# Kernel optimization log

Hardware: AMD Instinct MI355X
Metric: run time of the kernel (lower is better)

## Reference

```python
import jax, jax.numpy as jnp
import numpy as np

N = 200000      # active voxels
K = 27          # kernel volume (3x3x3)
M = 50000       # rulebook pairs per kernel offset
CIN = 64
COUT = 64


def setup_inputs() -> dict:
    key = jax.random.key(0)
    k1, k2, k3, k4 = jax.random.split(key, 4)
    feats = jax.random.normal(k1, (N, CIN), dtype=jnp.float32)
    std = 1.0 / np.sqrt(CIN * K)
    kernel = jax.random.uniform(k2, (K, CIN, COUT), dtype=jnp.float32,
                                minval=-std, maxval=std)
    in_map = jax.random.randint(k3, (K, M), 0, N, dtype=jnp.int32)
    out_map = jax.random.randint(k4, (K, M), 0, N, dtype=jnp.int32)
    return {"feats": feats, "kernel": kernel, "in_map": in_map, "out_map": out_map}


def reference(feats, kernel, in_map, out_map):
    # gather: [K, M, Cin]
    gathered = feats[in_map]
    # per-offset GEMM: [K, M, Cout]
    partial = jnp.einsum('kmi,kio->kmo', gathered, kernel)
    # scatter-add into output features [N, Cout]
    out = jnp.zeros((feats.shape[0], kernel.shape[-1]), dtype=feats.dtype)
    out = out.at[out_map].add(partial)
    return out
```

## Files before the change

kernel.cpp:

```cpp
#include <hip/hip_runtime.h>
#include <hip/hip_fp16.h>

#define CIN   64
#define COUT  64

typedef __attribute__((ext_vector_type(8))) short bf16x8;
typedef __attribute__((ext_vector_type(4))) float f32x4;
typedef __attribute__((ext_vector_type(4))) unsigned u32x4;

__device__ inline unsigned short f2bf(float f) {
    unsigned u = __float_as_uint(f);
    return (unsigned short)((u + 0x7FFFu + ((u >> 16) & 1u)) >> 16);
}

__device__ inline unsigned pack_h2(float lo, float hi) {
    __half l = __float2half(lo), h = __float2half(hi);
    return (unsigned)__half_as_ushort(l) | ((unsigned)__half_as_ushort(h) << 16);
}

__device__ inline float2 h2f2(unsigned v) {
    return make_float2(
        __half2float(__ushort_as_half((unsigned short)(v & 0xFFFFu))),
        __half2float(__ushort_as_half((unsigned short)(v >> 16))));
}

__global__ __launch_bounds__(256)
void cvt_hist(const f32x4* __restrict__ in, unsigned short* __restrict__ outb,
              int n8, const int* __restrict__ out_map, int total,
              int* __restrict__ cnt, int* __restrict__ rk) {
    int i = blockIdx.x * 256 + threadIdx.x;
    if (i < n8) {
        f32x4 f0 = __builtin_nontemporal_load(&in[2 * i]);
        f32x4 f1 = __builtin_nontemporal_load(&in[2 * i + 1]);
        bf16x8 o;
        o[0] = (short)f2bf(f0[0]); o[1] = (short)f2bf(f0[1]);
        o[2] = (short)f2bf(f0[2]); o[3] = (short)f2bf(f0[3]);
        o[4] = (short)f2bf(f1[0]); o[5] = (short)f2bf(f1[1]);
        o[6] = (short)f2bf(f1[2]); o[7] = (short)f2bf(f1[3]);
        *(bf16x8*)(outb + 8 * (size_t)i) = o;
    }
    if (i < total)
        rk[i] = atomicAdd(&cnt[out_map[i]], 1);
}

__global__ __launch_bounds__(256)
void scanA(const int* __restrict__ cnt, int* __restrict__ excl,
           int* __restrict__ blocksum, int N) {
    __shared__ int sm[256];
    const int b = blockIdx.x, t = threadIdx.x;
    const int base = b * 1024 + t * 4;
    int v0 = (base + 0 < N) ? cnt[base + 0] : 0;
    int v1 = (base + 1 < N) ? cnt[base + 1] : 0;
    int v2 = (base + 2 < N) ? cnt[base + 2] : 0;
    int v3 = (base + 3 < N) ? cnt[base + 3] : 0;
    const int s = v0 + v1 + v2 + v3;
    sm[t] = s; __syncthreads();
    for (int off = 1; off < 256; off <<= 1) {
        int x = (t >= off) ? sm[t - off] : 0;
        __syncthreads();
        sm[t] += x;
        __syncthreads();
    }
    const int e = sm[t] - s;
    if (t == 255) blocksum[b] = sm[t];
    if (base + 0 < N) excl[base + 0] = e;
    if (base + 1 < N) excl[base + 1] = e + v0;
    if (base + 2 < N) excl[base + 2] = e + v0 + v1;
    if (base + 3 < N) excl[base + 3] = e + v0 + v1 + v2;
}

__global__ __launch_bounds__(256)
void scanB(const int* __restrict__ blocksum, int* __restrict__ blockbase,
           int nb, int* __restrict__ total_out) {
    __shared__ int sm[256];
    const int t = threadIdx.x;
    const int s = (t < nb) ? blocksum[t] : 0;
    sm[t] = s; __syncthreads();
    for (int off = 1; off < 256; off <<= 1) {
        int x = (t >= off) ? sm[t - off] : 0;
        __syncthreads();
        sm[t] += x;
        __syncthreads();
    }
    if (t < nb) blockbase[t] = sm[t] - s;
    if (t == 255) *total_out = sm[255];
}

__global__ __launch_bounds__(256)
void scanC(int* __restrict__ offsets, const int* __restrict__ blockbase, int N,
           int nblk, const float* __restrict__ weight,
           unsigned short* __restrict__ wb, int kvol) {
    const int b = blockIdx.x;
    if (b < nblk) {
        int i = b * 256 + threadIdx.x;
        if (i < N) offsets[i] += blockbase[i >> 10];
        return;
    }
    const int idx = (b - nblk) * 256 + threadIdx.x;
    if (idx >= kvol * 64 * 8) return;
    const int k   = idx >> 9;
    const int rem = idx & 511;
    const int n   = rem >> 3;
    const int c0  = (rem & 7) << 3;
    const float* __restrict__ wk = weight + (size_t)k * (CIN * COUT);
    unsigned short* __restrict__ dst = wb + ((size_t)k * 64 + n) * 64 + c0;
#pragma unroll
    for (int j = 0; j < 8; ++j)
        dst[j] = f2bf(wk[(c0 + j) * COUT + n]);
}

__global__ __launch_bounds__(256)
void fill_idx(const int* __restrict__ out_map, const int* __restrict__ rk,
              const int* __restrict__ offsets, int* __restrict__ idx,
              int total) {
    int p = blockIdx.x * 256 + threadIdx.x;
    if (p < total)
        idx[offsets[out_map[p]] + rk[p]] = p;
}

__global__ __launch_bounds__(256)
void spconv_phase1(const unsigned short* __restrict__ featsb,
                   const unsigned short* __restrict__ wb,
                   const int*            __restrict__ in_map,
                   unsigned*             __restrict__ partial_dw,
                   int M) {
    const int k      = blockIdx.y;
    const int tid    = threadIdx.x;
    const int lane   = tid & 63;
    const int m      = lane & 15;
    const int quad   = lane >> 4;
    const int wave   = blockIdx.x * 4 + (tid >> 6);
    const int nwaves = gridDim.x * 4;

    const unsigned short* __restrict__ wkb = wb + (size_t)k * (CIN * COUT);
    bf16x8 afrag[4][2];
#pragma unroll
    for (int t = 0; t < 4; ++t) {
        const int n = 16 * (m >> 2) + 4 * t + (m & 3);
#pragma unroll
        for (int h = 0; h < 2; ++h)
            afrag[t][h] = *(const bf16x8*)(wkb + n * 64 + 32 * h + 8 * quad);
    }

    const int base   = k * M;
    const int ntiles = M >> 4;

    int t0 = wave, t1 = wave + nwaves, t2 = wave + 2 * nwaves;

    int ir0 = 0;
    if (t0 < ntiles) ir0 = in_map[base + (t0 << 4) + m];
    bf16x8 a0_0 = {}, a1_0 = {};
    if (t0 < ntiles) {
        const unsigned short* fb = featsb + ((size_t)ir0 << 6) + 8 * quad;
        a0_0 = *(const bf16x8*)fb;
        a1_0 = *(const bf16x8*)(fb + 32);
    }
    int ir1 = 0;
    if (t1 < ntiles) ir1 = in_map[base + (t1 << 4) + m];

    while (t0 < ntiles) {
        bf16x8 a0_1 = {}, a1_1 = {};
        if (t1 < ntiles) {
            const unsigned short* fb = featsb + ((size_t)ir1 << 6) + 8 * quad;
            a0_1 = *(const bf16x8*)fb;
            a1_1 = *(const bf16x8*)(fb + 32);
        }
        int ir2 = 0;
        if (t2 < ntiles) ir2 = in_map[base + (t2 << 4) + m];

        f32x4 acc[4];
#pragma unroll
        for (int t = 0; t < 4; ++t) {
            acc[t] = {0.f, 0.f, 0.f, 0.f};
            acc[t] = __builtin_amdgcn_mfma_f32_16x16x32_bf16(afrag[t][0], a0_0, acc[t], 0, 0, 0);
            acc[t] = __builtin_amdgcn_mfma_f32_16x16x32_bf16(afrag[t][1], a1_0, acc[t], 0, 0, 0);
        }

        const size_t pair = (size_t)base + ((size_t)t0 << 4) + m;
        unsigned d[8];
#pragma unroll
        for (int t = 0; t < 4; ++t) {
            d[2 * t]     = pack_h2(acc[t][0], acc[t][1]);
            d[2 * t + 1] = pack_h2(acc[t][2], acc[t][3]);
        }
        uint4* dst = (uint4*)(partial_dw + pair * 32 + 8 * quad);
        dst[0] = make_uint4(d[0], d[1], d[2], d[3]);
        dst[1] = make_uint4(d[4], d[5], d[6], d[7]);

        t0 = t1; t1 = t2; t2 += nwaves;
        a0_0 = a0_1; a1_0 = a1_1;
        ir1 = ir2;
    }
}

__global__ __launch_bounds__(256)
void spconv_phase2(const u32x4* __restrict__ partial_q,
                   const int*   __restrict__ idx,
                   const int*   __restrict__ offsets,
                   float4*      __restrict__ out4,
                   int nrows) {
    const int tid  = threadIdx.x;
    const int lane = tid & 63;
    const int g    = lane >> 3;
    const int q    = lane & 7;
    const int wave = blockIdx.x * 4 + (tid >> 6);
    const int nw   = gridDim.x * 4;

    for (int r0 = 4 * wave; r0 < nrows; r0 += 4 * nw) {
        const int nr = (nrows - r0 < 4) ? (nrows - r0) : 4;

        int offv[5];
        offv[0] = offsets[r0];
#pragma unroll
        for (int u = 1; u <= 4; ++u)
            offv[u] = (u <= nr) ? offsets[r0 + u] : offv[u - 1];

        int  pj[4];
        bool act[4];
#pragma unroll
        for (int u = 0; u < 4; ++u) {
            const int s = offv[u] + g;
            act[u] = (s < offv[u + 1]);
            pj[u]  = act[u] ? idx[s] : 0;
        }
        u32x4 v[4];
#pragma unroll
        for (int u = 0; u < 4; ++u) {
            v[u] = (u32x4){0u, 0u, 0u, 0u};
            if (act[u]) v[u] = partial_q[(size_t)pj[u] * 8 + q];
        }

        float acc[4][8];
#pragma unroll
        for (int u = 0; u < 4; ++u) {
            const float2 f0 = h2f2(v[u][0]), f1 = h2f2(v[u][1]);
            const float2 f2 = h2f2(v[u][2]), f3 = h2f2(v[u][3]);
            acc[u][0] = f0.x; acc[u][1] = f0.y; acc[u][2] = f1.x; acc[u][3] = f1.y;
            acc[u][4] = f2.x; acc[u][5] = f2.y; acc[u][6] = f3.x; acc[u][7] = f3.y;
        }

#pragma unroll
        for (int u = 0; u < 4; ++u) {
            const int cu = offv[u + 1] - offv[u];
            for (int j0 = 8; j0 < cu; j0 += 8) {
                const int j = j0 + g;
                if (j < cu) {
                    const int pj2 = idx[offv[u] + j];
                    const u32x4 w = partial_q[(size_t)pj2 * 8 + q];
                    const float2 f0 = h2f2(w[0]), f1 = h2f2(w[1]);
                    const float2 f2 = h2f2(w[2]), f3 = h2f2(w[3]);
                    acc[u][0] += f0.x; acc[u][1] += f0.y;
                    acc[u][2] += f1.x; acc[u][3] += f1.y;
                    acc[u][4] += f2.x; acc[u][5] += f2.y;
                    acc[u][6] += f3.x; acc[u][7] += f3.y;
                }
            }
        }

#pragma unroll
        for (int u = 0; u < 4; ++u)
#pragma unroll
            for (int e = 0; e < 8; ++e) {
                acc[u][e] += __shfl_xor(acc[u][e], 8);
                acc[u][e] += __shfl_xor(acc[u][e], 16);
                acc[u][e] += __shfl_xor(acc[u][e], 32);
            }

        if (g == 0) {
#pragma unroll
            for (int u = 0; u < 4; ++u) {
                if (u < nr) {
                    out4[(size_t)(r0 + u) * 16 + 2 * q] =
                        make_float4(acc[u][0], acc[u][1], acc[u][2], acc[u][3]);
                    out4[(size_t)(r0 + u) * 16 + 2 * q + 1] =
                        make_float4(acc[u][4], acc[u][5], acc[u][6], acc[u][7]);
                }
            }
        }
    }
}

__global__ __launch_bounds__(256)
void spconv_atomic(const float* __restrict__ feats,
                   const float* __restrict__ weight,
                   const int*   __restrict__ in_map,
                   const int*   __restrict__ out_map,
                   float*       __restrict__ out,
                   int M) {
    const int k      = blockIdx.y;
    const int tid    = threadIdx.x;
    const int lane   = tid & 63;
    const int m      = lane & 15;
    const int quad   = lane >> 4;
    const int wave   = blockIdx.x * 4 + (tid >> 6);
    const int nwaves = gridDim.x * 4;

    const float* __restrict__ wk = weight + (size_t)k * (CIN * COUT);
    bf16x8 bfrag[4][2];
#pragma unroll
    for (int t = 0; t < 4; ++t)
#pragma unroll
        for (int h = 0; h < 2; ++h) {
            const int n  = 16 * t + m;
            const int c0 = 32 * h + 8 * quad;
#pragma unroll
            for (int j = 0; j < 8; ++j)
                bfrag[t][h][j] = (short)f2bf(wk[(c0 + j) * COUT + n]);
        }

    const int base   = k * M;
    const int ntiles = M >> 4;

    for (int tile = wave; tile < ntiles; tile += nwaves) {
        const int p0 = tile << 4;
        const int in_row  = in_map[base + p0 + m];
        const int out_row = out_map[base + p0 + m];

        const float* __restrict__ fr = feats + ((size_t)in_row << 6) + 8 * quad;
        const f32x4 f0 = *(const f32x4*)(fr + 0);
        const f32x4 f1 = *(const f32x4*)(fr + 4);
        const f32x4 f2 = *(const f32x4*)(fr + 32);
        const f32x4 f3 = *(const f32x4*)(fr + 36);

        bf16x8 a0, a1;
#pragma unroll
        for (int j = 0; j < 4; ++j) {
            a0[j]     = (short)f2bf(f0[j]);
            a0[j + 4] = (short)f2bf(f1[j]);
            a1[j]     = (short)f2bf(f2[j]);
            a1[j + 4] = (short)f2bf(f3[j]);
        }

        int orow[4];
#pragma unroll
        for (int r = 0; r < 4; ++r)
            orow[r] = __shfl(out_row, 4 * quad + r);

        f32x4 acc[4];
#pragma unroll
        for (int t = 0; t < 4; ++t) {
            acc[t] = {0.f, 0.f, 0.f, 0.f};
            acc[t] = __builtin_amdgcn_mfma_f32_16x16x32_bf16(a0, bfrag[t][0], acc[t], 0, 0, 0);
            acc[t] = __builtin_amdgcn_mfma_f32_16x16x32_bf16(a1, bfrag[t][1], acc[t], 0, 0, 0);
        }

#pragma unroll
        for (int t = 0; t < 4; ++t)
#pragma unroll
            for (int r = 0; r < 4; ++r)
                atomicAdd(out + (size_t)orow[r] * COUT + 16 * t + m, acc[t][r]);
    }
}

__global__ __launch_bounds__(256)
void zero_out_kernel(float4* __restrict__ out, int n4) {
    int i = blockIdx.x * 256 + threadIdx.x;
    if (i < n4) out[i] = make_float4(0.f, 0.f, 0.f, 0.f);
}

static inline size_t al256(size_t x) { return (x + 255) & ~(size_t)255; }

extern "C" void kernel_launch(void* const* d_in, const int* in_sizes, int n_in,
                              void* d_out, int out_size, void* d_ws, size_t ws_size,
                              hipStream_t stream) {
    const float* feats   = (const float*)d_in[0];
    const float* weight  = (const float*)d_in[1];
    const int*   in_map  = (const int*)d_in[2];
    const int*   out_map = (const int*)d_in[3];
    float*       out     = (float*)d_out;

    const int K     = in_sizes[1] / (CIN * COUT);
    const int M     = in_sizes[2] / K;
    const int N     = out_size / COUT;
    const int total = K * M;
    const int nb    = (N + 1023) >> 10;

    const size_t off_b  = al256((size_t)(N + 1) * 4);
    const size_t cnt_b  = al256((size_t)N * 4);
    const size_t bs_b   = al256((size_t)nb * 4);
    const size_t bb_b   = al256((size_t)nb * 4);
    const size_t rank_b = al256((size_t)total * 4);
    const size_t idx_b  = al256((size_t)total * 4);
    const size_t wb_b   = al256((size_t)K * CIN * COUT * 2);
    const size_t fb_b   = al256((size_t)N * CIN * 2);
    const size_t part_b = (size_t)total * COUT * 2;
    const size_t need   = off_b + cnt_b + bs_b + bb_b + rank_b + idx_b
                        + wb_b + fb_b + part_b;

    if ((M & 15) == 0 && nb <= 256 && ws_size >= need) {
        char* p = (char*)d_ws;
        int*            offsets   = (int*)p;            p += off_b;
        int*            cnt       = (int*)p;            p += cnt_b;
        int*            blocksum  = (int*)p;            p += bs_b;
        int*            blockbase = (int*)p;            p += bb_b;
        int*            rk        = (int*)p;            p += rank_b;
        int*            idx       = (int*)p;            p += idx_b;
        unsigned short* wb        = (unsigned short*)p; p += wb_b;
        unsigned short* featsb    = (unsigned short*)p; p += fb_b;
        unsigned*       partial   = (unsigned*)p;

        const int n8 = N * CIN / 8;
        const int fused_n = (n8 > total) ? n8 : total;

        (void)hipMemsetAsync(cnt, 0, (size_t)N * 4, stream);
        cvt_hist<<<(fused_n + 255) / 256, 256, 0, stream>>>(
            (const f32x4*)feats, featsb, n8, out_map, total, cnt, rk);
        scanA<<<nb, 256, 0, stream>>>(cnt, offsets, blocksum, N);
        scanB<<<1, 256, 0, stream>>>(blocksum, blockbase, nb, offsets + N);

        const int nblkC = (N + 255) / 256;
        const int nwblk = (K * 64 * 8 + 255) / 256;
        scanC<<<nblkC + nwblk, 256, 0, stream>>>(offsets, blockbase, N,
                                                 nblkC, weight, wb, K);
        fill_idx<<<(total + 255) / 256, 256, 0, stream>>>(out_map, rk, offsets,
                                                          idx, total);

        dim3 g1(80, K);
        spconv_phase1<<<g1, 256, 0, stream>>>(featsb, wb, in_map, partial, M);

        spconv_phase2<<<8192, 256, 0, stream>>>((const u32x4*)partial, idx,
                                                offsets, (float4*)out, N);
        return;
    }

    int n4 = out_size / 4;
    zero_out_kernel<<<(n4 + 255) / 256, 256, 0, stream>>>((float4*)out, n4);
    dim3 grid(80, K);
    spconv_atomic<<<grid, 256, 0, stream>>>(feats, weight, in_map, out_map, out, M);
}
```

Measured before the change: 303.4 us.

## Fold block-base scan fixup into consumers and use nontemporal streaming accesses

Removes the separate pass that added block bases to the per-row offsets; fill_idx and phase2 now combine the exclusive scan and block base on the fly, and weight conversion runs in its own small kernel. Streaming reads of in_map, rank, idx and partials, and the partial stores, use nontemporal hints to reduce cache pollution. Phase2's grid is shrunk to one block per 1024 rows so each wave loops over more rows, trading parallelism and latency hiding for less launch and scheduling overhead.

```diff
diff --git a/kernel.cpp b/kernel.cpp
--- a/kernel.cpp
+++ b/kernel.cpp
@@ -71,7 +71,7 @@
 
 __global__ __launch_bounds__(256)
 void scanB(const int* __restrict__ blocksum, int* __restrict__ blockbase,
-           int nb, int* __restrict__ total_out) {
+           int nb) {
     __shared__ int sm[256];
     const int t = threadIdx.x;
     const int s = (t < nb) ? blocksum[t] : 0;
@@ -83,20 +83,13 @@
         __syncthreads();
     }
     if (t < nb) blockbase[t] = sm[t] - s;
-    if (t == 255) *total_out = sm[255];
-}
-
-__global__ __launch_bounds__(256)
-void scanC(int* __restrict__ offsets, const int* __restrict__ blockbase, int N,
-           int nblk, const float* __restrict__ weight,
-           unsigned short* __restrict__ wb, int kvol) {
-    const int b = blockIdx.x;
-    if (b < nblk) {
-        int i = b * 256 + threadIdx.x;
-        if (i < N) offsets[i] += blockbase[i >> 10];
-        return;
-    }
-    const int idx = (b - nblk) * 256 + threadIdx.x;
+    if (t == 255) blockbase[nb] = sm[255];
+}
+
+__global__ __launch_bounds__(256)
+void wconv(const float* __restrict__ weight, unsigned short* __restrict__ wb,
+           int kvol) {
+    const int idx = blockIdx.x * 256 + threadIdx.x;
     if (idx >= kvol * 64 * 8) return;
     const int k   = idx >> 9;
     const int rem = idx & 511;
@@ -111,11 +104,14 @@
 
 __global__ __launch_bounds__(256)
 void fill_idx(const int* __restrict__ out_map, const int* __restrict__ rk,
-              const int* __restrict__ offsets, int* __restrict__ idx,
-              int total) {
+              const int* __restrict__ excl, const int* __restrict__ bb,
+              int* __restrict__ idx, int total) {
     int p = blockIdx.x * 256 + threadIdx.x;
-    if (p < total)
-        idx[offsets[out_map[p]] + rk[p]] = p;
+    if (p < total) {
+        const int row = out_map[p];
+        const int r   = __builtin_nontemporal_load(&rk[p]);
+        idx[excl[row] + bb[row >> 10] + r] = p;
+    }
 }
 
 __global__ __launch_bounds__(256)
@@ -148,7 +144,7 @@
     int t0 = wave, t1 = wave + nwaves, t2 = wave + 2 * nwaves;
 
     int ir0 = 0;
-    if (t0 < ntiles) ir0 = in_map[base + (t0 << 4) + m];
+    if (t0 < ntiles) ir0 = __builtin_nontemporal_load(&in_map[base + (t0 << 4) + m]);
     bf16x8 a0_0 = {}, a1_0 = {};
     if (t0 < ntiles) {
         const unsigned short* fb = featsb + ((size_t)ir0 << 6) + 8 * quad;
@@ -156,7 +152,7 @@
         a1_0 = *(const bf16x8*)(fb + 32);
     }
     int ir1 = 0;
-    if (t1 < ntiles) ir1 = in_map[base + (t1 << 4) + m];
+    if (t1 < ntiles) ir1 = __builtin_nontemporal_load(&in_map[base + (t1 << 4) + m]);
 
     while (t0 < ntiles) {
         bf16x8 a0_1 = {}, a1_1 = {};
@@ -166,7 +162,7 @@
             a1_1 = *(const bf16x8*)(fb + 32);
         }
         int ir2 = 0;
-        if (t2 < ntiles) ir2 = in_map[base + (t2 << 4) + m];
+        if (t2 < ntiles) ir2 = __builtin_nontemporal_load(&in_map[base + (t2 << 4) + m]);
 
         f32x4 acc[4];
 #pragma unroll
@@ -177,15 +173,18 @@
         }
 
         const size_t pair = (size_t)base + ((size_t)t0 << 4) + m;
-        unsigned d[8];
-#pragma unroll
-        for (int t = 0; t < 4; ++t) {
-            d[2 * t]     = pack_h2(acc[t][0], acc[t][1]);
-            d[2 * t + 1] = pack_h2(acc[t][2], acc[t][3]);
-        }
-        uint4* dst = (uint4*)(partial_dw + pair * 32 + 8 * quad);
-        dst[0] = make_uint4(d[0], d[1], d[2], d[3]);
-        dst[1] = make_uint4(d[4], d[5], d[6], d[7]);
+        u32x4 w0, w1;
+        w0[0] = pack_h2(acc[0][0], acc[0][1]);
+        w0[1] = pack_h2(acc[0][2], acc[0][3]);
+        w0[2] = pack_h2(acc[1][0], acc[1][1]);
+        w0[3] = pack_h2(acc[1][2], acc[1][3]);
+        w1[0] = pack_h2(acc[2][0], acc[2][1]);
+        w1[1] = pack_h2(acc[2][2], acc[2][3]);
+        w1[2] = pack_h2(acc[3][0], acc[3][1]);
+        w1[3] = pack_h2(acc[3][2], acc[3][3]);
+        unsigned* bp = partial_dw + pair * 32 + 8 * quad;
+        __builtin_nontemporal_store(w0, (u32x4*)bp);
+        __builtin_nontemporal_store(w1, (u32x4*)(bp + 4));
 
         t0 = t1; t1 = t2; t2 += nwaves;
         a0_0 = a0_1; a1_0 = a1_1;
@@ -196,7 +195,9 @@
 __global__ __launch_bounds__(256)
 void spconv_phase2(const u32x4* __restrict__ partial_q,
                    const int*   __restrict__ idx,
-                   const int*   __restrict__ offsets,
+                   const int*   __restrict__ excl,
+                   const int*   __restrict__ bb,
+                   int nbq,
                    float4*      __restrict__ out4,
                    int nrows) {
     const int tid  = threadIdx.x;
@@ -205,15 +206,22 @@
     const int q    = lane & 7;
     const int wave = blockIdx.x * 4 + (tid >> 6);
     const int nw   = gridDim.x * 4;
+    const int tot  = bb[nbq];
 
     for (int r0 = 4 * wave; r0 < nrows; r0 += 4 * nw) {
         const int nr = (nrows - r0 < 4) ? (nrows - r0) : 4;
 
         int offv[5];
-        offv[0] = offsets[r0];
-#pragma unroll
-        for (int u = 1; u <= 4; ++u)
-            offv[u] = (u <= nr) ? offsets[r0 + u] : offv[u - 1];
+        offv[0] = excl[r0] + bb[r0 >> 10];
+#pragma unroll
+        for (int u = 1; u <= 4; ++u) {
+            if (u <= nr) {
+                const int i = r0 + u;
+                offv[u] = (i < nrows) ? (excl[i] + bb[i >> 10]) : tot;
+            } else {
+                offv[u] = offv[u - 1];
+            }
+        }
 
         int  pj[4];
         bool act[4];
@@ -221,13 +229,14 @@
         for (int u = 0; u < 4; ++u) {
             const int s = offv[u] + g;
             act[u] = (s < offv[u + 1]);
-            pj[u]  = act[u] ? idx[s] : 0;
+            pj[u]  = act[u] ? __builtin_nontemporal_load(&idx[s]) : 0;
         }
         u32x4 v[4];
 #pragma unroll
         for (int u = 0; u < 4; ++u) {
             v[u] = (u32x4){0u, 0u, 0u, 0u};
-            if (act[u]) v[u] = partial_q[(size_t)pj[u] * 8 + q];
+            if (act[u])
+                v[u] = __builtin_nontemporal_load(&partial_q[(size_t)pj[u] * 8 + q]);
         }
 
         float acc[4][8];
@@ -245,8 +254,9 @@
             for (int j0 = 8; j0 < cu; j0 += 8) {
                 const int j = j0 + g;
                 if (j < cu) {
-                    const int pj2 = idx[offv[u] + j];
-                    const u32x4 w = partial_q[(size_t)pj2 * 8 + q];
+                    const int pj2 = __builtin_nontemporal_load(&idx[offv[u] + j]);
+                    const u32x4 w = __builtin_nontemporal_load(
+                        &partial_q[(size_t)pj2 * 8 + q]);
                     const float2 f0 = h2f2(w[0]), f1 = h2f2(w[1]);
                     const float2 f2 = h2f2(w[2]), f3 = h2f2(w[3]);
                     acc[u][0] += f0.x; acc[u][1] += f0.y;
@@ -375,10 +385,10 @@
     const int total = K * M;
     const int nb    = (N + 1023) >> 10;
 
-    const size_t off_b  = al256((size_t)(N + 1) * 4);
+    const size_t off_b  = al256((size_t)N * 4);
     const size_t cnt_b  = al256((size_t)N * 4);
     const size_t bs_b   = al256((size_t)nb * 4);
-    const size_t bb_b   = al256((size_t)nb * 4);
+    const size_t bb_b   = al256((size_t)(nb + 1) * 4);
     const size_t rank_b = al256((size_t)total * 4);
     const size_t idx_b  = al256((size_t)total * 4);
     const size_t wb_b   = al256((size_t)K * CIN * COUT * 2);
@@ -389,7 +399,7 @@
 
     if ((M & 15) == 0 && nb <= 256 && ws_size >= need) {
         char* p = (char*)d_ws;
-        int*            offsets   = (int*)p;            p += off_b;
+        int*            excl      = (int*)p;            p += off_b;
         int*            cnt       = (int*)p;            p += cnt_b;
         int*            blocksum  = (int*)p;            p += bs_b;
         int*            blockbase = (int*)p;            p += bb_b;
@@ -405,21 +415,19 @@
         (void)hipMemsetAsync(cnt, 0, (size_t)N * 4, stream);
         cvt_hist<<<(fused_n + 255) / 256, 256, 0, stream>>>(
             (const f32x4*)feats, featsb, n8, out_map, total, cnt, rk);
-        scanA<<<nb, 256, 0, stream>>>(cnt, offsets, blocksum, N);
-        scanB<<<1, 256, 0, stream>>>(blocksum, blockbase, nb, offsets + N);
-
-        const int nblkC = (N + 255) / 256;
-        const int nwblk = (K * 64 * 8 + 255) / 256;
-        scanC<<<nblkC + nwblk, 256, 0, stream>>>(offsets, blockbase, N,
-                                                 nblkC, weight, wb, K);
-        fill_idx<<<(total + 255) / 256, 256, 0, stream>>>(out_map, rk, offsets,
-                                                          idx, total);
+        scanA<<<nb, 256, 0, stream>>>(cnt, excl, blocksum, N);
+        scanB<<<1, 256, 0, stream>>>(blocksum, blockbase, nb);
+        wconv<<<(K * 64 * 8 + 255) / 256, 256, 0, stream>>>(weight, wb, K);
+        fill_idx<<<(total + 255) / 256, 256, 0, stream>>>(out_map, rk, excl,
+                                                          blockbase, idx, total);
 
         dim3 g1(80, K);
         spconv_phase1<<<g1, 256, 0, stream>>>(featsb, wb, in_map, partial, M);
 
-        spconv_phase2<<<8192, 256, 0, stream>>>((const u32x4*)partial, idx,
-                                                offsets, (float4*)out, N);
+        const int g2 = (N + 1023) / 1024;
+        spconv_phase2<<<g2, 256, 0, stream>>>((const u32x4*)partial, idx,
+                                              excl, blockbase, nb,
+                                              (float4*)out, N);
         return;
     }
 
```

After: 570.9 us. 88.2% more time.
